# Kernel optimization log

Measured on AMD Instinct MI355X. Metric: run time of the kernel, lower is better.

Reference implementation:

```python
import jax, jax.numpy as jnp
import numpy as np

B, T, I, H, L, O = 256, 336, 16, 512, 256, 10


def setup_inputs() -> dict:
    key = jax.random.key(0)
    ks = jax.random.split(key, 24)
    n = lambda k, s, sc=1.0: jax.random.normal(k, s, dtype=jnp.float32) * sc
    mask = lambda k, s: (jax.random.uniform(k, s) > 0.5).astype(jnp.float32) * 2.0  # dropout p=0.5
    return {
        "x": n(ks[0], (B, T, I)),
        # dropout masks (inverted-dropout scaling already applied)
        "drop_x": mask(ks[1], (B, T, I)),
        "drop_h": mask(ks[2], (B, H)),
        "drop_l": mask(ks[3], (B, L)),
        # BayesianLSTM variational params + reparameterization noise
        "wih_mu": n(ks[4], (I, 4 * H), 0.05), "wih_rho": jnp.full((I, 4 * H), -5.0, jnp.float32), "eps_wih": n(ks[5], (I, 4 * H)),
        "whh_mu": n(ks[6], (H, 4 * H), 0.05), "whh_rho": jnp.full((H, 4 * H), -5.0, jnp.float32), "eps_whh": n(ks[7], (H, 4 * H)),
        "b_mu": n(ks[8], (4 * H,), 0.05), "b_rho": jnp.full((4 * H,), -5.0, jnp.float32), "eps_b": n(ks[9], (4 * H,)),
        # BayesianLinear variational params + noise (weight is [out, in])
        "blw_mu": n(ks[10], (L, H), 0.05), "blw_rho": jnp.full((L, H), -5.0, jnp.float32), "eps_blw": n(ks[11], (L, H)),
        "blb_mu": n(ks[12], (L,), 0.05), "blb_rho": jnp.full((L,), -5.0, jnp.float32), "eps_blb": n(ks[13], (L,)),
        # final deterministic linear, no bias
        "lin_w": n(ks[14], (O, L), 0.05),
    }


def _forward(x, drop_x, drop_h, drop_l,
             wih_mu, wih_rho, eps_wih, whh_mu, whh_rho, eps_whh,
             b_mu, b_rho, eps_b, blw_mu, blw_rho, eps_blw,
             blb_mu, blb_rho, eps_blb, lin_w):
    sp = jax.nn.softplus
    # sample weights: w = mu + softplus(rho) * eps
    Wih = wih_mu + sp(wih_rho) * eps_wih        # [I, 4H]
    Whh = whh_mu + sp(whh_rho) * eps_whh        # [H, 4H]
    b = b_mu + sp(b_rho) * eps_b                # [4H]
    BLW = blw_mu + sp(blw_rho) * eps_blw        # [L, H]
    BLb = blb_mu + sp(blb_rho) * eps_blb        # [L]

    xd = x * drop_x                             # dropout on input
    # precompute input-to-gate projection for all timesteps: [B, T, 4H]
    xg = jnp.einsum('bti,ig->btg', xd, Wih) + b

    def step(carry, xg_t):
        h, c = carry
        gates = xg_t + h @ Whh                  # [B, 4H]
        i, f, g, o = jnp.split(gates, 4, axis=-1)
        i = jax.nn.sigmoid(i)
        f = jax.nn.sigmoid(f)
        g = jnp.tanh(g)
        o = jax.nn.sigmoid(o)
        c = f * c + i * g
        h = o * jnp.tanh(c)
        return (h, c), h

    h0 = jnp.zeros((x.shape[0], Whh.shape[0]), x.dtype)
    (_, _), hs = jax.lax.scan(step, (h0, h0), jnp.swapaxes(xg, 0, 1))  # hs: [T, B, H]
    hidden_seq = jnp.swapaxes(hs, 0, 1)         # blitz returns batch-major [B, T, H]
    # faithful to lstm_out.view(sequence_length, len(x), hidden_dim)[-1] (reshape, not transpose)
    last = hidden_seq.reshape(T, x.shape[0], -1)[-1]    # [B, H]

    y = jax.nn.relu((last * drop_h) @ BLW.T + BLb)      # Bayesian linear + ReLU
    return (y * drop_l) @ lin_w.T                       # final linear, no bias


def reference(x, drop_x, drop_h, drop_l,
              wih_mu, wih_rho, eps_wih, whh_mu, whh_rho, eps_whh,
              b_mu, b_rho, eps_b, blw_mu, blw_rho, eps_blw,
              blb_mu, blb_rho, eps_blb, lin_w):
    return _forward(x, drop_x, drop_h, drop_l,
                    wih_mu, wih_rho, eps_wih, whh_mu, whh_rho, eps_whh,
                    b_mu, b_rho, eps_b, blw_mu, blw_rho, eps_blw,
                    blb_mu, blb_rho, eps_blb, lin_w)
```

## Files before the change

kernel.cpp:

```cpp
#include <hip/hip_runtime.h>

#define T_STEPS 336
#define NWG 32

typedef unsigned long long u64;

__device__ float g_h[337 * 512];
__device__ float g_blw[256 * 512];
__device__ float g_blb[256];
__device__ u64   g_hh[2][512];

__device__ __forceinline__ float softplus_f(float x) {
  return (x > 20.f) ? x : log1pf(__expf(x));
}
__device__ __forceinline__ float sigmoid_f(float x) {
  return 1.f / (1.f + __expf(-x));
}
__device__ __forceinline__ float tanh_f(float x) {
  x = fminf(fmaxf(x, -15.f), 15.f);
  float e = __expf(-2.f * x);
  return (1.f - e) / (1.f + e);
}

__global__ __launch_bounds__(256) void prep_kernel(
    const float* __restrict__ blw_mu, const float* __restrict__ blw_rho, const float* __restrict__ eps_blw,
    const float* __restrict__ blb_mu, const float* __restrict__ blb_rho, const float* __restrict__ eps_blb)
{
  const int bid = blockIdx.x, tid = threadIdx.x;
  if (bid < 512) {
    const int e = bid * 256 + tid;
    g_blw[e] = blw_mu[e] + softplus_f(blw_rho[e]) * eps_blw[e];
  } else {
    g_blb[tid] = blb_mu[tid] + softplus_f(blb_rho[tid]) * eps_blb[tid];
    u64* p = &g_hh[0][0];
    #pragma unroll
    for (int q = 0; q < 4; ++q)
      __hip_atomic_store(p + q * 256 + tid, 0ULL, __ATOMIC_RELAXED,
                         __HIP_MEMORY_SCOPE_AGENT);
  }
}

__global__ __launch_bounds__(512) void lstm_kernel(
    const float* __restrict__ x, const float* __restrict__ drop_x,
    const float* __restrict__ wih_mu, const float* __restrict__ wih_rho, const float* __restrict__ eps_wih,
    const float* __restrict__ b_mu, const float* __restrict__ b_rho, const float* __restrict__ eps_b,
    const float* __restrict__ whh_mu, const float* __restrict__ whh_rho, const float* __restrict__ eps_whh)
{
  const int r = blockIdx.x;
  const int tid = threadIdx.x;
  const int cl = tid & 63;
  const int seg = tid >> 6;
  const int gate = cl >> 4, kl = cl & 15;
  const int col = gate * 512 + r * 16 + kl;
  const int row0 = seg * 64;

  __shared__ float xd[336 * 16];
  __shared__ float hs[512];
  __shared__ float part[2][8][64];

  for (int e = tid; e < 5376; e += 512) {
    const int src = 255 * 5376 + e;
    xd[e] = x[src] * drop_x[src];
  }

  float w[64];
  #pragma unroll
  for (int j = 0; j < 64; ++j) {
    const int idx = (row0 + j) * 2048 + col;
    w[j] = whh_mu[idx] + softplus_f(whh_rho[idx]) * eps_whh[idx];
  }

  float wih[16];
  float bias = 0.f;
  if (tid < 64) {
    bias = b_mu[col] + softplus_f(b_rho[col]) * eps_b[col];
    #pragma unroll
    for (int i = 0; i < 16; ++i) {
      const int idx = i * 2048 + col;
      wih[i] = wih_mu[idx] + softplus_f(wih_rho[idx]) * eps_wih[idx];
    }
  }
  __syncthreads();

  float c = 0.f;

  for (int t = 0; t < T_STEPS; ++t) {
    const int p = t & 1;

    float xgv = 0.f;
    if (tid < 64) {
      const float4* xr = (const float4*)(xd + t * 16);
      float4 x0 = xr[0], x1 = xr[1], x2 = xr[2], x3 = xr[3];
      float s0 = fmaf(x0.x, wih[0], bias);
      s0 = fmaf(x0.y, wih[1], s0); s0 = fmaf(x0.z, wih[2], s0); s0 = fmaf(x0.w, wih[3], s0);
      float s1 = x1.x * wih[4];
      s1 = fmaf(x1.y, wih[5], s1); s1 = fmaf(x1.z, wih[6], s1); s1 = fmaf(x1.w, wih[7], s1);
      float s2 = x2.x * wih[8];
      s2 = fmaf(x2.y, wih[9], s2); s2 = fmaf(x2.z, wih[10], s2); s2 = fmaf(x2.w, wih[11], s2);
      float s3 = x3.x * wih[12];
      s3 = fmaf(x3.y, wih[13], s3); s3 = fmaf(x3.z, wih[14], s3); s3 = fmaf(x3.w, wih[15], s3);
      xgv = (s0 + s1) + (s2 + s3);
    }

    {
      const u64* slot = &g_hh[p][tid];
      u64 v;
      do {
        v = __hip_atomic_load(slot, __ATOMIC_RELAXED, __HIP_MEMORY_SCOPE_AGENT);
      } while ((unsigned)(v >> 32) != (unsigned)t);
      hs[tid] = __uint_as_float((unsigned)v);
    }

    float a0 = 0.f, a1 = 0.f, a2 = 0.f, a3 = 0.f;
    const float4* hv = (const float4*)(hs + row0);
    #pragma unroll
    for (int jj = 0; jj < 16; ++jj) {
      float4 h4 = hv[jj];
      a0 = fmaf(h4.x, w[4 * jj],     a0);
      a1 = fmaf(h4.y, w[4 * jj + 1], a1);
      a2 = fmaf(h4.z, w[4 * jj + 2], a2);
      a3 = fmaf(h4.w, w[4 * jj + 3], a3);
    }
    part[p][seg][cl] = (a0 + a1) + (a2 + a3);
    __syncthreads();

    if (tid < 64) {
      float g = xgv
              + ((part[p][0][tid] + part[p][1][tid]) + (part[p][2][tid] + part[p][3][tid]))
              + ((part[p][4][tid] + part[p][5][tid]) + (part[p][6][tid] + part[p][7][tid]));
      float vi = __shfl(g, kl);
      float vf = __shfl(g, kl + 16);
      float vg = __shfl(g, kl + 32);
      float vo = __shfl(g, kl + 48);
      if (tid < 16) {
        float ig = sigmoid_f(vi);
        float fg = sigmoid_f(vf);
        float gg = tanh_f(vg);
        float og = sigmoid_f(vo);
        c = fg * c + ig * gg;
        float h = og * tanh_f(c);
        g_h[(t + 1) * 512 + r * 16 + tid] = h;
        u64 pv = (((u64)(unsigned)(t + 1)) << 32) | (u64)__float_as_uint(h);
        __hip_atomic_store(&g_hh[(t + 1) & 1][r * 16 + tid], pv,
                           __ATOMIC_RELAXED, __HIP_MEMORY_SCOPE_AGENT);
      }
    }
  }
}

__global__ __launch_bounds__(256) void head_kernel(
    const float* __restrict__ drop_h, const float* __restrict__ drop_l,
    const float* __restrict__ lin_w, float* __restrict__ out)
{
  const int j = blockIdx.x, tid = threadIdx.x;
  __shared__ float hd[512];
  __shared__ float y[256];

  for (int k = tid; k < 512; k += 256)
    hd[k] = g_h[(81 + j) * 512 + k] * drop_h[j * 512 + k];
  __syncthreads();

  {
    const int l = tid;
    float acc = g_blb[l];
    const float* wrow = g_blw + l * 512;
    #pragma unroll 8
    for (int k = 0; k < 512; ++k) acc = fmaf(hd[k], wrow[k], acc);
    acc = fmaxf(acc, 0.f);
    y[l] = acc * drop_l[j * 256 + l];
  }
  __syncthreads();

  if (tid < 10) {
    float acc = 0.f;
    const float* lrow = lin_w + tid * 256;
    #pragma unroll 8
    for (int l = 0; l < 256; ++l) acc = fmaf(y[l], lrow[l], acc);
    out[j * 10 + tid] = acc;
  }
}

extern "C" void kernel_launch(void* const* d_in, const int* in_sizes, int n_in,
                              void* d_out, int out_size, void* d_ws, size_t ws_size,
                              hipStream_t stream) {
  const float* x        = (const float*)d_in[0];
  const float* drop_x   = (const float*)d_in[1];
  const float* drop_h   = (const float*)d_in[2];
  const float* drop_l   = (const float*)d_in[3];
  const float* wih_mu   = (const float*)d_in[4];
  const float* wih_rho  = (const float*)d_in[5];
  const float* eps_wih  = (const float*)d_in[6];
  const float* whh_mu   = (const float*)d_in[7];
  const float* whh_rho  = (const float*)d_in[8];
  const float* eps_whh  = (const float*)d_in[9];
  const float* b_mu     = (const float*)d_in[10];
  const float* b_rho    = (const float*)d_in[11];
  const float* eps_b    = (const float*)d_in[12];
  const float* blw_mu   = (const float*)d_in[13];
  const float* blw_rho  = (const float*)d_in[14];
  const float* eps_blw  = (const float*)d_in[15];
  const float* blb_mu   = (const float*)d_in[16];
  const float* blb_rho  = (const float*)d_in[17];
  const float* eps_blb  = (const float*)d_in[18];
  const float* lin_w    = (const float*)d_in[19];

  prep_kernel<<<513, 256, 0, stream>>>(blw_mu, blw_rho, eps_blw,
                                       blb_mu, blb_rho, eps_blb);

  lstm_kernel<<<NWG, 512, 0, stream>>>(x, drop_x,
                                       wih_mu, wih_rho, eps_wih,
                                       b_mu, b_rho, eps_b,
                                       whh_mu, whh_rho, eps_whh);

  head_kernel<<<256, 256, 0, stream>>>(drop_h, drop_l, lin_w, (float*)d_out);
}
```

Baseline: 726.4 us.

## Co-locate recurrent LSTM workgroups on one XCD and poll hidden state via sc0 loads

The kernel now launches 256 workgroups, and each reads its hardware XCD id and draws a per-XCD ticket. The first XCD to collect 32 workgroups wins, its members run the recurrence and all other workgroups exit. Keeping the 32 cooperating workgroups on one XCD lets them exchange the hidden state through the shared L2 using sc0 loads and stores, instead of agent-scope atomics that cross dies. The change also stores h in fp16 in shared memory and computes the next step's input projection early. The risks are lower precision in the recurrent dot product, a spin loop that gives up after a bounded number of tries (possible wrong results), and a dependence on hardware register layout and dispatch behaviour.

```diff
diff --git a/kernel.cpp b/kernel.cpp
--- a/kernel.cpp
+++ b/kernel.cpp
@@ -1,7 +1,9 @@
 #include <hip/hip_runtime.h>
+#include <hip/hip_fp16.h>
 
 #define T_STEPS 336
 #define NWG 32
+#define LAUNCH_WGS 256
 
 typedef unsigned long long u64;
 
@@ -9,6 +11,8 @@
 __device__ float g_blw[256 * 512];
 __device__ float g_blb[256];
 __device__ u64   g_hh[2][512];
+__device__ int   g_tick[8];
+__device__ int   g_winner;
 
 __device__ __forceinline__ float softplus_f(float x) {
   return (x > 20.f) ? x : log1pf(__expf(x));
@@ -20,6 +24,16 @@
   x = fminf(fmaxf(x, -15.f), 15.f);
   float e = __expf(-2.f * x);
   return (1.f - e) / (1.f + e);
+}
+
+__device__ __forceinline__ u64 load_sc0(const u64* p) {
+  u64 v;
+  asm volatile("global_load_dwordx2 %0, %1, off sc0\n\ts_waitcnt vmcnt(0)"
+               : "=v"(v) : "v"(p) : "memory");
+  return v;
+}
+__device__ __forceinline__ void store_sc0(u64* p, u64 v) {
+  asm volatile("global_store_dwordx2 %0, %1, off sc0" :: "v"(p), "v"(v) : "memory");
 }
 
 __global__ __launch_bounds__(256) void prep_kernel(
@@ -37,6 +51,10 @@
     for (int q = 0; q < 4; ++q)
       __hip_atomic_store(p + q * 256 + tid, 0ULL, __ATOMIC_RELAXED,
                          __HIP_MEMORY_SCOPE_AGENT);
+    if (tid < 8)
+      __hip_atomic_store(&g_tick[tid], 0, __ATOMIC_RELAXED, __HIP_MEMORY_SCOPE_AGENT);
+    if (tid == 8)
+      __hip_atomic_store(&g_winner, -1, __ATOMIC_RELAXED, __HIP_MEMORY_SCOPE_AGENT);
   }
 }
 
@@ -46,17 +64,41 @@
     const float* __restrict__ b_mu, const float* __restrict__ b_rho, const float* __restrict__ eps_b,
     const float* __restrict__ whh_mu, const float* __restrict__ whh_rho, const float* __restrict__ eps_whh)
 {
-  const int r = blockIdx.x;
   const int tid = threadIdx.x;
+
+  __shared__ int s_role;
+  if (tid == 0) {
+    const int xcd = __builtin_amdgcn_s_getreg(6164) & 7;
+    const int ticket = __hip_atomic_fetch_add(&g_tick[xcd], 1,
+                          __ATOMIC_RELAXED, __HIP_MEMORY_SCOPE_AGENT);
+    int role = -1;
+    if (ticket < NWG) {
+      if (ticket == NWG - 1) {
+        int exp = -1;
+        __hip_atomic_compare_exchange_strong(&g_winner, &exp, xcd,
+            __ATOMIC_RELAXED, __ATOMIC_RELAXED, __HIP_MEMORY_SCOPE_AGENT);
+      }
+      int wv;
+      do {
+        wv = __hip_atomic_load(&g_winner, __ATOMIC_RELAXED, __HIP_MEMORY_SCOPE_AGENT);
+      } while (wv == -1);
+      if (wv == xcd) role = ticket;
+    }
+    s_role = role;
+  }
+  __syncthreads();
+  const int r = s_role;
+  if (r < 0) return;
+
   const int cl = tid & 63;
   const int seg = tid >> 6;
   const int gate = cl >> 4, kl = cl & 15;
   const int col = gate * 512 + r * 16 + kl;
   const int row0 = seg * 64;
 
-  __shared__ float xd[336 * 16];
-  __shared__ float hs[512];
-  __shared__ float part[2][8][64];
+  __shared__ float  xd[336 * 16];
+  __shared__ __half hs16[512];
+  __shared__ float  part[2][8][64];
 
   for (int e = tid; e < 5376; e += 512) {
     const int src = 255 * 5376 + e;
@@ -82,44 +124,59 @@
   }
   __syncthreads();
 
+  auto xg_at = [&](int t) -> float {
+    const float4* xr = (const float4*)(xd + t * 16);
+    float4 x0 = xr[0], x1 = xr[1], x2 = xr[2], x3 = xr[3];
+    float s0 = fmaf(x0.x, wih[0], bias);
+    s0 = fmaf(x0.y, wih[1], s0); s0 = fmaf(x0.z, wih[2], s0); s0 = fmaf(x0.w, wih[3], s0);
+    float s1 = x1.x * wih[4];
+    s1 = fmaf(x1.y, wih[5], s1); s1 = fmaf(x1.z, wih[6], s1); s1 = fmaf(x1.w, wih[7], s1);
+    float s2 = x2.x * wih[8];
+    s2 = fmaf(x2.y, wih[9], s2); s2 = fmaf(x2.z, wih[10], s2); s2 = fmaf(x2.w, wih[11], s2);
+    float s3 = x3.x * wih[12];
+    s3 = fmaf(x3.y, wih[13], s3); s3 = fmaf(x3.z, wih[14], s3); s3 = fmaf(x3.w, wih[15], s3);
+    return (s0 + s1) + (s2 + s3);
+  };
+
   float c = 0.f;
+  float xgv = (tid < 64) ? xg_at(0) : 0.f;
 
   for (int t = 0; t < T_STEPS; ++t) {
     const int p = t & 1;
 
-    float xgv = 0.f;
-    if (tid < 64) {
-      const float4* xr = (const float4*)(xd + t * 16);
-      float4 x0 = xr[0], x1 = xr[1], x2 = xr[2], x3 = xr[3];
-      float s0 = fmaf(x0.x, wih[0], bias);
-      s0 = fmaf(x0.y, wih[1], s0); s0 = fmaf(x0.z, wih[2], s0); s0 = fmaf(x0.w, wih[3], s0);
-      float s1 = x1.x * wih[4];
-      s1 = fmaf(x1.y, wih[5], s1); s1 = fmaf(x1.z, wih[6], s1); s1 = fmaf(x1.w, wih[7], s1);
-      float s2 = x2.x * wih[8];
-      s2 = fmaf(x2.y, wih[9], s2); s2 = fmaf(x2.z, wih[10], s2); s2 = fmaf(x2.w, wih[11], s2);
-      float s3 = x3.x * wih[12];
-      s3 = fmaf(x3.y, wih[13], s3); s3 = fmaf(x3.z, wih[14], s3); s3 = fmaf(x3.w, wih[15], s3);
-      xgv = (s0 + s1) + (s2 + s3);
-    }
-
     {
-      const u64* slot = &g_hh[p][tid];
+      u64* slot = &g_hh[p][tid];
       u64 v;
-      do {
-        v = __hip_atomic_load(slot, __ATOMIC_RELAXED, __HIP_MEMORY_SCOPE_AGENT);
-      } while ((unsigned)(v >> 32) != (unsigned)t);
-      hs[tid] = __uint_as_float((unsigned)v);
+      for (int it = 0; ; ++it) {
+        v = load_sc0(slot);
+        if ((unsigned)(v >> 32) == (unsigned)t) break;
+        if ((it & 3) == 3) {
+          v = __hip_atomic_load(slot, __ATOMIC_RELAXED, __HIP_MEMORY_SCOPE_AGENT);
+          if ((unsigned)(v >> 32) == (unsigned)t) break;
+          if (it > (1 << 18)) break;
+        }
+      }
+      hs16[tid] = __float2half(__uint_as_float((unsigned)v));
     }
 
     float a0 = 0.f, a1 = 0.f, a2 = 0.f, a3 = 0.f;
-    const float4* hv = (const float4*)(hs + row0);
+    const float4* hv = (const float4*)(hs16 + row0);
     #pragma unroll
-    for (int jj = 0; jj < 16; ++jj) {
-      float4 h4 = hv[jj];
-      a0 = fmaf(h4.x, w[4 * jj],     a0);
-      a1 = fmaf(h4.y, w[4 * jj + 1], a1);
-      a2 = fmaf(h4.z, w[4 * jj + 2], a2);
-      a3 = fmaf(h4.w, w[4 * jj + 3], a3);
+    for (int jj = 0; jj < 8; ++jj) {
+      float4 q = hv[jj];
+      const __half2* hp = (const __half2*)&q;
+      float2 f0 = __half22float2(hp[0]);
+      float2 f1 = __half22float2(hp[1]);
+      float2 f2 = __half22float2(hp[2]);
+      float2 f3 = __half22float2(hp[3]);
+      a0 = fmaf(f0.x, w[8 * jj],     a0);
+      a1 = fmaf(f0.y, w[8 * jj + 1], a1);
+      a2 = fmaf(f1.x, w[8 * jj + 2], a2);
+      a3 = fmaf(f1.y, w[8 * jj + 3], a3);
+      a0 = fmaf(f2.x, w[8 * jj + 4], a0);
+      a1 = fmaf(f2.y, w[8 * jj + 5], a1);
+      a2 = fmaf(f3.x, w[8 * jj + 6], a2);
+      a3 = fmaf(f3.y, w[8 * jj + 7], a3);
     }
     part[p][seg][cl] = (a0 + a1) + (a2 + a3);
     __syncthreads();
@@ -139,11 +196,14 @@
         float og = sigmoid_f(vo);
         c = fg * c + ig * gg;
         float h = og * tanh_f(c);
-        g_h[(t + 1) * 512 + r * 16 + tid] = h;
+        const int idx = r * 16 + tid;
         u64 pv = (((u64)(unsigned)(t + 1)) << 32) | (u64)__float_as_uint(h);
-        __hip_atomic_store(&g_hh[(t + 1) & 1][r * 16 + tid], pv,
+        store_sc0(&g_hh[(t + 1) & 1][idx], pv);
+        __hip_atomic_store(&g_hh[(t + 1) & 1][idx], pv,
                            __ATOMIC_RELAXED, __HIP_MEMORY_SCOPE_AGENT);
+        g_h[(t + 1) * 512 + idx] = h;
       }
+      if (t + 1 < T_STEPS) xgv = xg_at(t + 1);
     }
   }
 }
@@ -207,10 +267,10 @@
   prep_kernel<<<513, 256, 0, stream>>>(blw_mu, blw_rho, eps_blw,
                                        blb_mu, blb_rho, eps_blb);
 
-  lstm_kernel<<<NWG, 512, 0, stream>>>(x, drop_x,
-                                       wih_mu, wih_rho, eps_wih,
-                                       b_mu, b_rho, eps_b,
-                                       whh_mu, whh_rho, eps_whh);
+  lstm_kernel<<<LAUNCH_WGS, 512, 0, stream>>>(x, drop_x,
+                                              wih_mu, wih_rho, eps_wih,
+                                              b_mu, b_rho, eps_b,
+                                              whh_mu, whh_rho, eps_whh);
 
   head_kernel<<<256, 256, 0, stream>>>(drop_h, drop_l, lin_w, (float*)d_out);
 }
```

Result: slower. 785.4 us (+8.1%).

## Store recurrent hidden state in fp16 shared memory and parallelize gate activations

Applied to the files above, without the earlier changes.

Hidden state is converted to half precision in shared memory, so each thread reads half as many bytes per step and unpacks them to float for the FMAs against fp32 weights. Gate activations now run across all 64 lanes, with tanh written as 2*sigmoid(2x)-1, before the shuffle, instead of 16 lanes each evaluating four activations serially. The input projection for the next step is computed after the current publish, taking it off the critical path, and the g_h store is moved after the atomic publish. It also adds a bounded spin loop. The fp16 rounding of h lowers accuracy, and a timeout break could silently continue with stale data.

```diff
diff --git a/kernel.cpp b/kernel.cpp
--- a/kernel.cpp
+++ b/kernel.cpp
@@ -1,4 +1,5 @@
 #include <hip/hip_runtime.h>
+#include <hip/hip_fp16.h>
 
 #define T_STEPS 336
 #define NWG 32
@@ -54,9 +55,9 @@
   const int col = gate * 512 + r * 16 + kl;
   const int row0 = seg * 64;
 
-  __shared__ float xd[336 * 16];
-  __shared__ float hs[512];
-  __shared__ float part[2][8][64];
+  __shared__ float  xd[336 * 16];
+  __shared__ __half hs16[512];
+  __shared__ float  part[2][8][64];
 
   for (int e = tid; e < 5376; e += 512) {
     const int src = 255 * 5376 + e;
@@ -82,44 +83,56 @@
   }
   __syncthreads();
 
+  auto xg_at = [&](int t) -> float {
+    const float4* xr = (const float4*)(xd + t * 16);
+    float4 x0 = xr[0], x1 = xr[1], x2 = xr[2], x3 = xr[3];
+    float s0 = fmaf(x0.x, wih[0], bias);
+    s0 = fmaf(x0.y, wih[1], s0); s0 = fmaf(x0.z, wih[2], s0); s0 = fmaf(x0.w, wih[3], s0);
+    float s1 = x1.x * wih[4];
+    s1 = fmaf(x1.y, wih[5], s1); s1 = fmaf(x1.z, wih[6], s1); s1 = fmaf(x1.w, wih[7], s1);
+    float s2 = x2.x * wih[8];
+    s2 = fmaf(x2.y, wih[9], s2); s2 = fmaf(x2.z, wih[10], s2); s2 = fmaf(x2.w, wih[11], s2);
+    float s3 = x3.x * wih[12];
+    s3 = fmaf(x3.y, wih[13], s3); s3 = fmaf(x3.z, wih[14], s3); s3 = fmaf(x3.w, wih[15], s3);
+    return (s0 + s1) + (s2 + s3);
+  };
+
   float c = 0.f;
+  float xgv = (tid < 64) ? xg_at(0) : 0.f;
 
   for (int t = 0; t < T_STEPS; ++t) {
     const int p = t & 1;
-
-    float xgv = 0.f;
-    if (tid < 64) {
-      const float4* xr = (const float4*)(xd + t * 16);
-      float4 x0 = xr[0], x1 = xr[1], x2 = xr[2], x3 = xr[3];
-      float s0 = fmaf(x0.x, wih[0], bias);
-      s0 = fmaf(x0.y, wih[1], s0); s0 = fmaf(x0.z, wih[2], s0); s0 = fmaf(x0.w, wih[3], s0);
-      float s1 = x1.x * wih[4];
-      s1 = fmaf(x1.y, wih[5], s1); s1 = fmaf(x1.z, wih[6], s1); s1 = fmaf(x1.w, wih[7], s1);
-      float s2 = x2.x * wih[8];
-      s2 = fmaf(x2.y, wih[9], s2); s2 = fmaf(x2.z, wih[10], s2); s2 = fmaf(x2.w, wih[11], s2);
-      float s3 = x3.x * wih[12];
-      s3 = fmaf(x3.y, wih[13], s3); s3 = fmaf(x3.z, wih[14], s3); s3 = fmaf(x3.w, wih[15], s3);
-      xgv = (s0 + s1) + (s2 + s3);
-    }
 
     {
       const u64* slot = &g_hh[p][tid];
       u64 v;
-      do {
+      int it = 0;
+      for (;;) {
         v = __hip_atomic_load(slot, __ATOMIC_RELAXED, __HIP_MEMORY_SCOPE_AGENT);
-      } while ((unsigned)(v >> 32) != (unsigned)t);
-      hs[tid] = __uint_as_float((unsigned)v);
+        if ((unsigned)(v >> 32) == (unsigned)t) break;
+        if (++it > (1 << 20)) break;
+      }
+      hs16[tid] = __float2half(__uint_as_float((unsigned)v));
     }
 
     float a0 = 0.f, a1 = 0.f, a2 = 0.f, a3 = 0.f;
-    const float4* hv = (const float4*)(hs + row0);
+    const float4* hv = (const float4*)(hs16 + row0);
     #pragma unroll
-    for (int jj = 0; jj < 16; ++jj) {
-      float4 h4 = hv[jj];
-      a0 = fmaf(h4.x, w[4 * jj],     a0);
-      a1 = fmaf(h4.y, w[4 * jj + 1], a1);
-      a2 = fmaf(h4.z, w[4 * jj + 2], a2);
-      a3 = fmaf(h4.w, w[4 * jj + 3], a3);
+    for (int jj = 0; jj < 8; ++jj) {
+      float4 q = hv[jj];
+      const __half2* hp = (const __half2*)&q;
+      float2 f0 = __half22float2(hp[0]);
+      float2 f1 = __half22float2(hp[1]);
+      float2 f2 = __half22float2(hp[2]);
+      float2 f3 = __half22float2(hp[3]);
+      a0 = fmaf(f0.x, w[8 * jj],     a0);
+      a1 = fmaf(f0.y, w[8 * jj + 1], a1);
+      a2 = fmaf(f1.x, w[8 * jj + 2], a2);
+      a3 = fmaf(f1.y, w[8 * jj + 3], a3);
+      a0 = fmaf(f2.x, w[8 * jj + 4], a0);
+      a1 = fmaf(f2.y, w[8 * jj + 5], a1);
+      a2 = fmaf(f3.x, w[8 * jj + 6], a2);
+      a3 = fmaf(f3.y, w[8 * jj + 7], a3);
     }
     part[p][seg][cl] = (a0 + a1) + (a2 + a3);
     __syncthreads();
@@ -128,22 +141,24 @@
       float g = xgv
               + ((part[p][0][tid] + part[p][1][tid]) + (part[p][2][tid] + part[p][3][tid]))
               + ((part[p][4][tid] + part[p][5][tid]) + (part[p][6][tid] + part[p][7][tid]));
-      float vi = __shfl(g, kl);
-      float vf = __shfl(g, kl + 16);
-      float vg = __shfl(g, kl + 32);
-      float vo = __shfl(g, kl + 48);
+      const bool is_g = (gate == 2);
+      float xin = is_g ? 2.f * fminf(fmaxf(g, -15.f), 15.f) : g;
+      float s = sigmoid_f(xin);
+      float act = is_g ? 2.f * s - 1.f : s;
+      float vi = __shfl(act, kl);
+      float vf = __shfl(act, kl + 16);
+      float vg = __shfl(act, kl + 32);
+      float vo = __shfl(act, kl + 48);
       if (tid < 16) {
-        float ig = sigmoid_f(vi);
-        float fg = sigmoid_f(vf);
-        float gg = tanh_f(vg);
-        float og = sigmoid_f(vo);
-        c = fg * c + ig * gg;
-        float h = og * tanh_f(c);
-        g_h[(t + 1) * 512 + r * 16 + tid] = h;
+        c = vf * c + vi * vg;
+        float h = vo * tanh_f(c);
+        const int idx = r * 16 + tid;
         u64 pv = (((u64)(unsigned)(t + 1)) << 32) | (u64)__float_as_uint(h);
-        __hip_atomic_store(&g_hh[(t + 1) & 1][r * 16 + tid], pv,
+        __hip_atomic_store(&g_hh[(t + 1) & 1][idx], pv,
                            __ATOMIC_RELAXED, __HIP_MEMORY_SCOPE_AGENT);
+        g_h[(t + 1) * 512 + idx] = h;
       }
+      if (t + 1 < T_STEPS) xgv = xg_at(t + 1);
     }
   }
 }
```

New measurement: 732.0 us. No clear change (+0.8%).
